# Kernel optimization log

Hardware: AMD Instinct MI355X
Metric: run time of the kernel (lower is better)

The kernel has to match this reference:

```python
import jax, jax.numpy as jnp
import numpy as np

N = 16384  # n_nodes
D = 64     # feature dim


def setup_inputs() -> dict:
    key = jax.random.key(0)
    kx, ka = jax.random.split(key)
    x = jax.random.normal(kx, (N, D), dtype=jnp.float32)
    # original code only tests adj[idx] == 1, so 0/1 int entries are faithful
    adj = jax.random.randint(ka, (N, N), 0, 2, dtype=jnp.int32)
    return {"x": x, "adj": adj}


def reference(x, adj):
    # GraphPool: for each node, sum its own feature vector plus the feature
    # vectors of all neighbors j with adj[i, j] == 1.
    # Vectorized: out = adj @ x + x  (dense binary SpMM + self term).
    a = (adj == 1).astype(x.dtype)  # [N, N]
    return jnp.matmul(a, x) + x     # [N, D]
```

## Files before the change

### kernel.cpp

```cpp
#include <hip/hip_runtime.h>

#define NN 16384
#define DD 64

typedef _Float16 f16x8 __attribute__((ext_vector_type(8)));
typedef short    s16x8 __attribute__((ext_vector_type(8)));
typedef float    f32x4 __attribute__((ext_vector_type(4)));
typedef int      i32x4 __attribute__((ext_vector_type(4)));

__global__ __launch_bounds__(256) void prep_x(const float* __restrict__ x,
                                              _Float16* __restrict__ ws) {
    int tid = blockIdx.x * 256 + threadIdx.x;
    int l  = tid & 63;
    int tc = tid >> 6;
    int c  = tc & 3;
    int t  = tc >> 2;
    int q  = l >> 4;
    int m  = l & 15;
    int row0 = t * 32 + q * 8;
    int col  = c * 16 + m;
    f16x8 v;
#pragma unroll
    for (int j = 0; j < 8; ++j)
        v[j] = (_Float16)x[(size_t)(row0 + j) * DD + col];
    *(f16x8*)(ws + (size_t)tid * 8) = v;
}

__global__ __launch_bounds__(256) void graphpool_gemm(const int* __restrict__ adj,
                                                      const float* __restrict__ x,
                                                      const _Float16* __restrict__ xs,
                                                      float* __restrict__ out) {
    __shared__ _Float16 sB[2][8192];

    const int tid = threadIdx.x;
    const int w   = tid >> 6;
    const int l   = tid & 63;
    const int q   = l >> 4;
    const int m   = l & 15;
    const int row16 = blockIdx.x * 64 + w * 16;

    const int* aptr = adj + (size_t)(row16 + m) * NN + q * 8;

    f32x4 acc[4];
#pragma unroll
    for (int c = 0; c < 4; ++c) acc[c] = (f32x4){0.f, 0.f, 0.f, 0.f};

    i32x4 areg[2][4][2];
    f16x8 sreg[4];

    auto loadA = [&](int n, int buf) {
#pragma unroll
        for (int s = 0; s < 4; ++s) {
            const i32x4* p = (const i32x4*)(aptr + (size_t)n * 128 + s * 32);
            areg[buf][s][0] = __builtin_nontemporal_load(p);
            areg[buf][s][1] = __builtin_nontemporal_load(p + 1);
        }
    };
    auto stageRead = [&](int n) {
        const f16x8* src = (const f16x8*)(xs + (size_t)n * 8192);
#pragma unroll
        for (int p = 0; p < 4; ++p) sreg[p] = src[p * 256 + tid];
    };
    auto stageWrite = [&](int buf) {
        f16x8* dst = (f16x8*)sB[buf];
#pragma unroll
        for (int p = 0; p < 4; ++p) dst[p * 256 + tid] = sreg[p];
    };

    stageRead(0);
    loadA(0, 0);
    stageWrite(0);
    __syncthreads();

    auto step = [&](int n, int buf, int nb) {
        const bool pf = (n + 1 < NN / 128);
        if (pf) { stageRead(n + 1); loadA(n + 1, nb); }
#pragma unroll
        for (int s = 0; s < 4; ++s) {
            int av[8];
            {
                i32x4 v0 = areg[buf][s][0], v1 = areg[buf][s][1];
                av[0] = v0.x; av[1] = v0.y; av[2] = v0.z; av[3] = v0.w;
                av[4] = v1.x; av[5] = v1.y; av[6] = v1.z; av[7] = v1.w;
            }
            s16x8 ai;
#pragma unroll
            for (int j = 0; j < 8; ++j)
                ai[j] = av[j] ? (short)0x3C00 : (short)0;
            f16x8 af = __builtin_bit_cast(f16x8, ai);
#pragma unroll
            for (int c = 0; c < 4; ++c) {
                f16x8 bf = *(const f16x8*)&sB[buf][((s * 4 + c) * 64 + l) * 8];
                acc[c] = __builtin_amdgcn_mfma_f32_16x16x32_f16(af, bf, acc[c], 0, 0, 0);
            }
        }
        if (pf) stageWrite(nb);
        __syncthreads();
    };

    for (int n = 0; n < NN / 128; n += 2) {
        step(n,     0, 1);
        step(n + 1, 1, 0);
    }

#pragma unroll
    for (int c = 0; c < 4; ++c) {
#pragma unroll
        for (int r = 0; r < 4; ++r) {
            int row = row16 + q * 4 + r;
            int col = c * 16 + m;
            size_t off = (size_t)row * DD + col;
            out[off] = acc[c][r] + x[off];
        }
    }
}

__global__ void graphpool_fallback(const int* __restrict__ adj,
                                   const float* __restrict__ x,
                                   float* __restrict__ out) {
    int i = blockIdx.x;
    int d = threadIdx.x;
    float acc = x[(size_t)i * DD + d];
    const int* row = adj + (size_t)i * NN;
    for (int j = 0; j < NN; ++j)
        if (row[j]) acc += x[(size_t)j * DD + d];
    out[(size_t)i * DD + d] = acc;
}

extern "C" void kernel_launch(void* const* d_in, const int* in_sizes, int n_in,
                              void* d_out, int out_size, void* d_ws, size_t ws_size,
                              hipStream_t stream) {
    const float* x   = (const float*)d_in[0];
    const int*   adj = (const int*)d_in[1];
    float*       out = (float*)d_out;

    const size_t ws_needed = (size_t)NN * DD * sizeof(_Float16);
    if (ws_size >= ws_needed) {
        _Float16* xs = (_Float16*)d_ws;
        prep_x<<<512, 256, 0, stream>>>(x, xs);
        graphpool_gemm<<<NN / 64, 256, 0, stream>>>(adj, x, xs, out);
    } else {
        graphpool_fallback<<<NN, 64, 0, stream>>>(adj, x, out);
    }
}
```

Baseline: 1.419 ms.

## Split GEMM along K into four partitions with a separate reduction kernel

The main GEMM grid is split four ways along the reduction dimension, giving 1024 blocks instead of 256 so more CUs have work on the bandwidth-bound adjacency stream. The B operand is now read directly from global memory (L2-resident) instead of being staged through shared memory with barriers. A new reduce_add kernel sums the four fp32 partials plus x. prep_x is also rewritten to coalesce its reads through shared memory. The cost is an extra 16 MB of partial-sum traffic and one more kernel launch.

Measured after the change: 1.772 ms. 24.8% more time.

```diff
diff --git a/kernel.cpp b/kernel.cpp
--- a/kernel.cpp
+++ b/kernel.cpp
@@ -10,43 +10,54 @@
 
 __global__ __launch_bounds__(256) void prep_x(const float* __restrict__ x,
                                               _Float16* __restrict__ ws) {
-    int tid = blockIdx.x * 256 + threadIdx.x;
-    int l  = tid & 63;
-    int tc = tid >> 6;
-    int c  = tc & 3;
-    int t  = tc >> 2;
-    int q  = l >> 4;
-    int m  = l & 15;
-    int row0 = t * 32 + q * 8;
-    int col  = c * 16 + m;
+    __shared__ float sx[32][65];
+    const int tid = threadIdx.x;
+    const int t   = blockIdx.x;
+
+    {
+        int r  = tid >> 3;
+        int c8 = (tid & 7) * 8;
+        const float* src = x + ((size_t)t * 32 + r) * DD + c8;
+        f32x4 a = *(const f32x4*)src;
+        f32x4 b = *(const f32x4*)(src + 4);
+#pragma unroll
+        for (int j = 0; j < 4; ++j) { sx[r][c8 + j] = a[j]; sx[r][c8 + 4 + j] = b[j]; }
+    }
+    __syncthreads();
+
+    const int l = tid & 63;
+    const int c = tid >> 6;
+    const int q = l >> 4;
+    const int m = l & 15;
     f16x8 v;
 #pragma unroll
     for (int j = 0; j < 8; ++j)
-        v[j] = (_Float16)x[(size_t)(row0 + j) * DD + col];
-    *(f16x8*)(ws + (size_t)tid * 8) = v;
+        v[j] = (_Float16)sx[q * 8 + j][c * 16 + m];
+    *(f16x8*)(ws + (((size_t)t * 256 + c * 64 + l) * 8)) = v;
 }
 
-__global__ __launch_bounds__(256) void graphpool_gemm(const int* __restrict__ adj,
-                                                      const float* __restrict__ x,
-                                                      const _Float16* __restrict__ xs,
-                                                      float* __restrict__ out) {
-    __shared__ _Float16 sB[2][8192];
-
+__global__ __launch_bounds__(256, 3) void graphpool_gemm(const int* __restrict__ adj,
+                                                         const _Float16* __restrict__ xs,
+                                                         float* __restrict__ part) {
     const int tid = threadIdx.x;
     const int w   = tid >> 6;
     const int l   = tid & 63;
     const int q   = l >> 4;
     const int m   = l & 15;
-    const int row16 = blockIdx.x * 64 + w * 16;
 
-    const int* aptr = adj + (size_t)(row16 + m) * NN + q * 8;
+    const int rb    = blockIdx.x >> 2;
+    const int kq    = blockIdx.x & 3;
+    const int row16 = rb * 64 + w * 16;
+    const int KQ    = NN / 4;
+
+    const int* aptr = adj + (size_t)(row16 + m) * NN + (size_t)kq * KQ + q * 8;
+    const f16x8* xv = (const f16x8*)xs + (size_t)kq * (KQ / 32) * 256 + l;
 
     f32x4 acc[4];
 #pragma unroll
     for (int c = 0; c < 4; ++c) acc[c] = (f32x4){0.f, 0.f, 0.f, 0.f};
 
     i32x4 areg[2][4][2];
-    f16x8 sreg[4];
 
     auto loadA = [&](int n, int buf) {
 #pragma unroll
@@ -56,25 +67,12 @@
             areg[buf][s][1] = __builtin_nontemporal_load(p + 1);
         }
     };
-    auto stageRead = [&](int n) {
-        const f16x8* src = (const f16x8*)(xs + (size_t)n * 8192);
-#pragma unroll
-        for (int p = 0; p < 4; ++p) sreg[p] = src[p * 256 + tid];
-    };
-    auto stageWrite = [&](int buf) {
-        f16x8* dst = (f16x8*)sB[buf];
-#pragma unroll
-        for (int p = 0; p < 4; ++p) dst[p * 256 + tid] = sreg[p];
-    };
 
-    stageRead(0);
+    constexpr int NCH = (NN / 4) / 128;
     loadA(0, 0);
-    stageWrite(0);
-    __syncthreads();
-
-    auto step = [&](int n, int buf, int nb) {
-        const bool pf = (n + 1 < NN / 128);
-        if (pf) { stageRead(n + 1); loadA(n + 1, nb); }
+    for (int n = 0; n < NCH; ++n) {
+        const int buf = n & 1;
+        if (n + 1 < NCH) loadA(n + 1, buf ^ 1);
 #pragma unroll
         for (int s = 0; s < 4; ++s) {
             int av[8];
@@ -88,31 +86,33 @@
             for (int j = 0; j < 8; ++j)
                 ai[j] = av[j] ? (short)0x3C00 : (short)0;
             f16x8 af = __builtin_bit_cast(f16x8, ai);
+            const f16x8* bp = xv + (size_t)(n * 4 + s) * 256;
 #pragma unroll
-            for (int c = 0; c < 4; ++c) {
-                f16x8 bf = *(const f16x8*)&sB[buf][((s * 4 + c) * 64 + l) * 8];
-                acc[c] = __builtin_amdgcn_mfma_f32_16x16x32_f16(af, bf, acc[c], 0, 0, 0);
-            }
+            for (int c = 0; c < 4; ++c)
+                acc[c] = __builtin_amdgcn_mfma_f32_16x16x32_f16(af, bp[c * 64], acc[c], 0, 0, 0);
         }
-        if (pf) stageWrite(nb);
-        __syncthreads();
-    };
-
-    for (int n = 0; n < NN / 128; n += 2) {
-        step(n,     0, 1);
-        step(n + 1, 1, 0);
     }
 
+    float* po = part + (size_t)kq * NN * DD;
 #pragma unroll
     for (int c = 0; c < 4; ++c) {
 #pragma unroll
         for (int r = 0; r < 4; ++r) {
-            int row = row16 + q * 4 + r;
-            int col = c * 16 + m;
-            size_t off = (size_t)row * DD + col;
-            out[off] = acc[c][r] + x[off];
+            size_t off = (size_t)(row16 + q * 4 + r) * DD + c * 16 + m;
+            __builtin_nontemporal_store(acc[c][r], po + off);
         }
     }
+}
+
+__global__ __launch_bounds__(256) void reduce_add(const float* __restrict__ part,
+                                                  const float* __restrict__ x,
+                                                  float* __restrict__ out) {
+    size_t i = (size_t)blockIdx.x * 256 + threadIdx.x;
+    f32x4 v = ((const f32x4*)x)[i];
+#pragma unroll
+    for (int g = 0; g < 4; ++g)
+        v += ((const f32x4*)(part + (size_t)g * NN * DD))[i];
+    ((f32x4*)out)[i] = v;
 }
 
 __global__ void graphpool_fallback(const int* __restrict__ adj,
@@ -134,11 +134,14 @@
     const int*   adj = (const int*)d_in[1];
     float*       out = (float*)d_out;
 
-    const size_t ws_needed = (size_t)NN * DD * sizeof(_Float16);
-    if (ws_size >= ws_needed) {
-        _Float16* xs = (_Float16*)d_ws;
+    const size_t xs_bytes   = (size_t)NN * DD * sizeof(_Float16);
+    const size_t part_bytes = (size_t)4 * NN * DD * sizeof(float);
+    if (ws_size >= xs_bytes + part_bytes) {
+        _Float16* xs   = (_Float16*)d_ws;
+        float*    part = (float*)((char*)d_ws + xs_bytes);
         prep_x<<<512, 256, 0, stream>>>(x, xs);
-        graphpool_gemm<<<NN / 64, 256, 0, stream>>>(adj, x, xs, out);
+        graphpool_gemm<<<1024, 256, 0, stream>>>(adj, xs, part);
+        reduce_add<<<1024, 256, 0, stream>>>(part, x, out);
     } else {
         graphpool_fallback<<<NN, 64, 0, stream>>>(adj, x, out);
     }
```
